# Optimization experiments

Measured on AMD Instinct MI355X. Metric: run time of the kernel, lower is better.

## Reference

```python
import jax, jax.numpy as jnp
import numpy as np

N = 50000
NEG_SLOPE = 0.2  # PyG GATConv default


def _add_self_loops(edge_index, n):
    loop = jnp.arange(n, dtype=edge_index.dtype)
    src = jnp.concatenate([edge_index[0], loop])
    dst = jnp.concatenate([edge_index[1], loop])
    return src, dst


def _gat_layer(x, src, dst, W, a_src, a_dst, b, concat):
    n = x.shape[0]
    H, C = a_src.shape
    h = (x @ W).reshape(n, H, C)                      # [N,H,C]
    s_src = jnp.sum(h * a_src, axis=-1)               # [N,H] per-node src score
    s_dst = jnp.sum(h * a_dst, axis=-1)               # [N,H] per-node dst score
    e = jax.nn.leaky_relu(s_src[src] + s_dst[dst], NEG_SLOPE)  # [E,H]
    m = jax.ops.segment_max(e, dst, num_segments=n)   # segment softmax (stable)
    ex = jnp.exp(e - m[dst])
    denom = jax.ops.segment_sum(ex, dst, num_segments=n)
    alpha = ex / denom[dst]                           # [E,H]
    out = jax.ops.segment_sum(h[src] * alpha[:, :, None], dst, num_segments=n)
    out = out.reshape(n, H * C) if concat else out.mean(axis=1)
    return out + b


def setup_inputs() -> dict:
    key = jax.random.key(0)
    ks = jax.random.split(key, 10)
    in_dim, hid, heads1, out_dim, heads2 = 256, 16, 8, 64, 1
    x = jax.random.normal(ks[0], (N, in_dim), dtype=jnp.float32)
    edge_index = jax.random.randint(ks[1], (2, 800000), 0, N, dtype=jnp.int64)
    sc1 = 1.0 / np.sqrt(in_dim)
    sc2 = 1.0 / np.sqrt(hid * heads1)
    W1 = jax.random.normal(ks[2], (in_dim, heads1 * hid), dtype=jnp.float32) * sc1
    a1_src = jax.random.normal(ks[3], (heads1, hid), dtype=jnp.float32) * sc1
    a1_dst = jax.random.normal(ks[4], (heads1, hid), dtype=jnp.float32) * sc1
    b1 = jnp.zeros((heads1 * hid,), dtype=jnp.float32)
    W2 = jax.random.normal(ks[5], (heads1 * hid, heads2 * out_dim), dtype=jnp.float32) * sc2
    a2_src = jax.random.normal(ks[6], (heads2, out_dim), dtype=jnp.float32) * sc2
    a2_dst = jax.random.normal(ks[7], (heads2, out_dim), dtype=jnp.float32) * sc2
    b2 = jnp.zeros((out_dim,), dtype=jnp.float32)
    return {"x": x, "edge_index": edge_index, "W1": W1, "a1_src": a1_src,
            "a1_dst": a1_dst, "b1": b1, "W2": W2, "a2_src": a2_src,
            "a2_dst": a2_dst, "b2": b2}


def reference(x, edge_index, W1, a1_src, a1_dst, b1, W2, a2_src, a2_dst, b2):
    # eval mode: dropout layers are identity
    src, dst = _add_self_loops(edge_index, x.shape[0])
    h = _gat_layer(x, src, dst, W1, a1_src, a1_dst, b1, concat=True)
    h = jax.nn.elu(h)
    out = _gat_layer(h, src, dst, W2, a2_src, a2_dst, b2, concat=False)
    return jax.nn.log_softmax(out, axis=1)
```

## Files before the change

### kernel.cpp

```cpp
#include <hip/hip_runtime.h>
#include <hip/hip_bf16.h>

typedef __attribute__((ext_vector_type(8))) short short8;
typedef __attribute__((ext_vector_type(4))) float f32x4;

#define EDGE_CHUNK 4096
#define CAP 128

__device__ __forceinline__ float lrelu(float v) { return fmaxf(v, 0.2f * v); }

__device__ __forceinline__ short bf16_hi(float f, float* back) {
    __hip_bfloat16 h = __float2bfloat16(f);
    *back = __bfloat162float(h);
    return __builtin_bit_cast(short, h);
}
__device__ __forceinline__ short f2bf(float f) {
    return __builtin_bit_cast(short, __float2bfloat16(f));
}


__device__ void packW_body(const float* __restrict__ W1, const float* __restrict__ a1s,
                           const float* __restrict__ a1d, const float* __restrict__ W2,
                           const float* __restrict__ a2s, const float* __restrict__ a2d,
                           short* __restrict__ w1hi, short* __restrict__ w1lo,
                           short* __restrict__ w2hi, short* __restrict__ w2lo, int t) {
    if (t < 256 * 144) {
        int j = t & 7, lane = (t >> 3) & 63, tile = t >> 9;
        int nt = tile % 9, kt = tile / 9;
        int k = kt * 32 + (lane >> 4) * 8 + j;
        int c = nt * 16 + (lane & 15);
        float w;
        if (c < 128) {
            w = W1[(size_t)k * 128 + c];
        } else {
            int hh = c - 128, h = hh & 7;
            const float* a = (hh >= 8) ? a1d : a1s;
            w = 0.f;
#pragma unroll
            for (int q = 0; q < 16; q++) w += W1[(size_t)k * 128 + h * 16 + q] * a[h * 16 + q];
        }
        float back;
        w1hi[t] = bf16_hi(w, &back);
        w1lo[t] = f2bf(w - back);
    } else {
        int u = t - 256 * 144;
        if (u >= 128 * 80) return;
        int j = u & 7, lane = (u >> 3) & 63, tile = u >> 9;
        int nt = tile % 5, kt = tile / 5;
        int k = kt * 32 + (lane >> 4) * 8 + j;
        int c = nt * 16 + (lane & 15);
        float w = 0.f;
        if (c < 64) {
            w = W2[(size_t)k * 64 + c];
        } else if (c < 66) {
            const float* a = (c == 65) ? a2d : a2s;
#pragma unroll
            for (int q = 0; q < 64; q++) w += W2[(size_t)k * 64 + q] * a[q];
        }
        float back;
        w2hi[u] = bf16_hi(w, &back);
        w2lo[u] = f2bf(w - back);
    }
}

__device__ void scatter_body(const int* __restrict__ ei, int E, int n,
                             int* __restrict__ cursor, int* __restrict__ csr_src, int vbid) {
    int slot = vbid & 7;
    int chunk = vbid >> 3;
    int lo = (int)(((long)n * slot) >> 3);
    int hi = (int)(((long)n * (slot + 1)) >> 3);
    int ET = E + n;
    int base = chunk * EDGE_CHUNK;
    int endi = min(base + EDGE_CHUNK, ET);
    for (int i = base + threadIdx.x; i < endi; i += 256) {
        int d = (i < E) ? ei[E + i] : i - E;
        if (d >= lo && d < hi) {
            int pos = atomicAdd(&cursor[d], 1);
            if (pos < CAP) {
                int s = (i < E) ? ei[i] : d;
                csr_src[(size_t)d * CAP + pos] = s;
            }
        }
    }
}

template <int K, int NT, int MODE>
__device__ void gemm_body(const float* __restrict__ A, const short* __restrict__ Bhi,
                          const short* __restrict__ Blo, unsigned short* __restrict__ hb,
                          float* __restrict__ s_s, float* __restrict__ s_d, int M, int vbid) {
    constexpr int KT = K / 32;
    constexpr int NH = NT - 1;
    __shared__ __align__(16) unsigned short stage[4][16][NH * 16];
    const int wave = threadIdx.x >> 6, lane = threadIdx.x & 63;
    const int row0 = (vbid * 4 + wave) * 16;
    if (row0 >= M) return;
    const int arow = row0 + (lane & 15);
    const float* ap = A + (size_t)arow * K + (lane >> 4) * 8;

    f32x4 acc[NT];
#pragma unroll
    for (int i = 0; i < NT; i++) acc[i] = (f32x4){0.f, 0.f, 0.f, 0.f};

    for (int kt = 0; kt < KT; kt++) {
        float av[8];
        *(float4*)(av)     = *(const float4*)(ap + kt * 32);
        *(float4*)(av + 4) = *(const float4*)(ap + kt * 32 + 4);
        short8 ahi, alo;
#pragma unroll
        for (int j = 0; j < 8; j++) {
            float back;
            ahi[j] = bf16_hi(av[j], &back);
            alo[j] = f2bf(av[j] - back);
        }
        const short8* bh = (const short8*)(Bhi + ((size_t)(kt * NT) * 64 + lane) * 8);
        const short8* bl = (const short8*)(Blo + ((size_t)(kt * NT) * 64 + lane) * 8);
#pragma unroll
        for (int nt = 0; nt < NT; nt++) {
            short8 bhv = bh[nt * 64];
            short8 blv = bl[nt * 64];
            acc[nt] = __builtin_amdgcn_mfma_f32_16x16x32_bf16(ahi, bhv, acc[nt], 0, 0, 0);
            acc[nt] = __builtin_amdgcn_mfma_f32_16x16x32_bf16(ahi, blv, acc[nt], 0, 0, 0);
            acc[nt] = __builtin_amdgcn_mfma_f32_16x16x32_bf16(alo, bhv, acc[nt], 0, 0, 0);
        }
    }
    const int rgrp = (lane >> 4) * 4;
    const int col = lane & 15;
#pragma unroll
    for (int nt = 0; nt < NH; nt++)
#pragma unroll
        for (int r = 0; r < 4; r++)
            stage[wave][rgrp + r][nt * 16 + col] = (unsigned short)f2bf(acc[nt][r]);
    asm volatile("s_waitcnt lgkmcnt(0)" ::: "memory");
    {
        const uint4* srcp = (const uint4*)&stage[wave][0][0];
        uint4* dstp = (uint4*)(hb + (size_t)row0 * (NH * 16));
#pragma unroll
        for (int c = lane; c < NH * 32; c += 64) dstp[c] = srcp[c];
    }
#pragma unroll
    for (int r = 0; r < 4; r++) {
        int orow = row0 + rgrp + r;
        float v = acc[NH][r];
        if (MODE == 1) {
            if (col < 8) s_s[orow * 8 + col] = v;
            else         s_d[orow * 8 + (col - 8)] = v;
        } else {
            if (col == 0)      s_s[orow] = v;
            else if (col == 1) s_d[orow] = v;
        }
    }
}


__launch_bounds__(256)
__global__ void fused_pack_scatter(const float* __restrict__ W1, const float* __restrict__ a1s,
                                   const float* __restrict__ a1d, const float* __restrict__ W2,
                                   const float* __restrict__ a2s, const float* __restrict__ a2d,
                                   short* __restrict__ w1hi, short* __restrict__ w1lo,
                                   short* __restrict__ w2hi, short* __restrict__ w2lo,
                                   const int* __restrict__ ei, int E, int n,
                                   int* __restrict__ cursor, int* __restrict__ csr_src,
                                   int npack) {
    if ((int)blockIdx.x < npack) {
        int t = blockIdx.x * 256 + threadIdx.x;
        packW_body(W1, a1s, a1d, W2, a2s, a2d, w1hi, w1lo, w2hi, w2lo, t);
    } else {
        scatter_body(ei, E, n, cursor, csr_src, blockIdx.x - npack);
    }
}

template <int K, int NT, int MODE>
__launch_bounds__(256)
__global__ void mfma_gemm(const float* __restrict__ A, const short* __restrict__ Bhi,
                          const short* __restrict__ Blo, unsigned short* __restrict__ hb,
                          float* __restrict__ s_s, float* __restrict__ s_d, int M) {
    gemm_body<K, NT, MODE>(A, Bhi, Blo, hb, s_s, s_d, M, blockIdx.x);
}

__launch_bounds__(256)
__global__ void gather1_kernel(const int* __restrict__ degv, const int* __restrict__ csr_src,
                               const float* __restrict__ ssrc, const float* __restrict__ sdst,
                               const unsigned short* __restrict__ h1b,
                               const float* __restrict__ b1, float* __restrict__ out1, int n) {
    int wid = blockIdx.x * 4 + (threadIdx.x >> 6);
    if (wid >= n) return;
    int lane = threadIdx.x & 63;
    int eg = lane >> 3;
    int hs = lane & 7;
    int ha = lane >> 3;
    float sd_s = sdst[wid * 8 + hs];
    int dg = degv[wid]; if (dg > CAP) dg = CAP;
    int beg = wid * CAP, end = beg + dg;
    float den_p = 0.f, a0 = 0.f, a1 = 0.f;

    int idx0 = beg + eg;
    int src_c = (idx0 < end) ? csr_src[idx0] : 0;
    int src_n = (idx0 + 8 < end) ? csr_src[idx0 + 8] : 0;
    float sc_c = (idx0 < end) ? ssrc[src_c * 8 + hs] : 0.f;

    for (int i = beg; i < end; i += 8) {
        int src_n2 = (i + 16 + eg < end) ? csr_src[i + 16 + eg] : 0;
        float sc_n = (i + 8 + eg < end) ? ssrc[src_n * 8 + hs] : 0.f;
        float e = (i + eg < end) ? __expf(lrelu(sc_c + sd_s)) : 0.f;
        den_p += e;
        int nn = end - i;
#define G1_BODY(k)                                                                  \
        {                                                                           \
            float eb = __shfl(e, (k) * 8 + ha, 64);                                 \
            int sb = __shfl(src_c, (k) * 8, 64);                                    \
            unsigned xw = *(const unsigned*)(h1b + (size_t)sb * 128 + 2 * lane);    \
            a0 = __builtin_fmaf(eb, __uint_as_float(xw << 16), a0);                 \
            a1 = __builtin_fmaf(eb, __uint_as_float(xw & 0xffff0000u), a1);         \
        }
        if (nn >= 8) {
#pragma unroll
            for (int k = 0; k < 8; k++) G1_BODY(k)
        } else {
            for (int k = 0; k < nn; k++) G1_BODY(k)
        }
#undef G1_BODY
        src_c = src_n; src_n = src_n2; sc_c = sc_n;
    }
    den_p += __shfl_xor(den_p, 8, 64);
    den_p += __shfl_xor(den_p, 16, 64);
    den_p += __shfl_xor(den_p, 32, 64);
    float den = __shfl(den_p, ha, 64);
    float inv = 1.f / den;
    float2 bb = *(const float2*)(b1 + 2 * lane);
    float o0 = __builtin_fmaf(a0, inv, bb.x);
    float o1 = __builtin_fmaf(a1, inv, bb.y);
    float2 o;
    o.x = o0 > 0.f ? o0 : (__expf(o0) - 1.f);
    o.y = o1 > 0.f ? o1 : (__expf(o1) - 1.f);
    *(float2*)(out1 + (size_t)wid * 128 + 2 * lane) = o;
}

__launch_bounds__(256)
__global__ void gather2_kernel(const int* __restrict__ degv, const int* __restrict__ csr_src,
                               const float* __restrict__ ssrc, const float* __restrict__ sdst,
                               const unsigned short* __restrict__ h2b,
                               const float* __restrict__ b2, float* __restrict__ out, int n) {
    int wid = blockIdx.x * 4 + (threadIdx.x >> 6);
    if (wid >= n) return;
    int lane = threadIdx.x & 63;
    float sd = sdst[wid];
    int dg = degv[wid]; if (dg > CAP) dg = CAP;
    int beg = wid * CAP, end = beg + dg;
    float den_p = 0.f, acc = 0.f;

    int idx0 = beg + lane;
    int src_c = (idx0 < end) ? csr_src[idx0] : 0;
    float sc_c = (idx0 < end) ? ssrc[src_c] : 0.f;

    for (int i = beg; i < end; i += 64) {
        float e = (i + lane < end) ? __expf(lrelu(sc_c + sd)) : 0.f;
        den_p += e;
        int nn = end - i; if (nn > 64) nn = 64;
#define G2_BODY(k)                                                                  \
        {                                                                           \
            float eb = __shfl(e, (k), 64);                                          \
            int sb = __shfl(src_c, (k), 64);                                        \
            float x = __uint_as_float(((unsigned)h2b[(size_t)sb * 64 + lane]) << 16);\
            acc = __builtin_fmaf(eb, x, acc);                                       \
        }
        int k = 0;
        for (; k + 8 <= nn; k += 8) {
#pragma unroll
            for (int u = 0; u < 8; u++) G2_BODY(k + u)
        }
        for (; k < nn; k++) G2_BODY(k)
#undef G2_BODY
        if (i + 64 < end) {
            int idx = i + 64 + lane;
            src_c = (idx < end) ? csr_src[idx] : 0;
            sc_c = (idx < end) ? ssrc[src_c] : 0.f;
        }
    }
#pragma unroll
    for (int off = 1; off < 64; off <<= 1) den_p += __shfl_xor(den_p, off, 64);

    float o = acc / den_p + b2[lane];
    float mx = o;
#pragma unroll
    for (int off = 32; off; off >>= 1) mx = fmaxf(mx, __shfl_xor(mx, off, 64));
    float ex = __expf(o - mx);
    float sum = ex;
#pragma unroll
    for (int off = 32; off; off >>= 1) sum += __shfl_xor(sum, off, 64);
    out[(size_t)wid * 64 + lane] = o - mx - logf(sum);
}

extern "C" void kernel_launch(void* const* d_in, const int* in_sizes, int n_in,
                              void* d_out, int out_size, void* d_ws, size_t ws_size,
                              hipStream_t stream) {
    const float* x   = (const float*)d_in[0];
    const int*   ei  = (const int*)d_in[1];
    const float* W1  = (const float*)d_in[2];
    const float* a1s = (const float*)d_in[3];
    const float* a1d = (const float*)d_in[4];
    const float* b1  = (const float*)d_in[5];
    const float* W2  = (const float*)d_in[6];
    const float* a2s = (const float*)d_in[7];
    const float* a2d = (const float*)d_in[8];
    const float* b2  = (const float*)d_in[9];
    float* out = (float*)d_out;

    const int n = in_sizes[0] / 256;
    const int E = in_sizes[1] / 2;
    const int ET = E + n;
    const int NCH = (ET + EDGE_CHUNK - 1) / EDGE_CHUNK;
    const int NPACK = (256 * 144 + 128 * 80) / 256;

    float* ws = (float*)d_ws;
    float* out1 = ws;
    float* s1s  = out1 + (size_t)n * 128;
    float* s1d  = s1s + (size_t)n * 8;
    float* s2s  = s1d + (size_t)n * 8;
    float* s2d  = s2s + n;
    unsigned short* h1b = (unsigned short*)(s2d + n);
    unsigned short* h2b = h1b + (size_t)n * 128;
    int*   cursor  = (int*)(h2b + (size_t)n * 64);
    int*   csr_src = cursor + n;
    short* w1hi    = (short*)(csr_src + (size_t)n * CAP);
    short* w1lo    = w1hi + 256 * 144;
    short* w2hi    = w1lo + 256 * 144;
    short* w2lo    = w2hi + 128 * 80;

    hipMemsetAsync(cursor, 0, (size_t)n * 4, stream);

    const int B = 256;

    fused_pack_scatter<<<NPACK + 8 * NCH, B, 0, stream>>>(W1, a1s, a1d, W2, a2s, a2d,
                                                          w1hi, w1lo, w2hi, w2lo,
                                                          ei, E, n, cursor, csr_src, NPACK);
    mfma_gemm<256, 9, 1><<<(n + 63) / 64, B, 0, stream>>>(x, w1hi, w1lo, h1b, s1s, s1d, n);
    gather1_kernel<<<(n + 3) / 4, B, 0, stream>>>(cursor, csr_src, s1s, s1d, h1b, b1, out1, n);
    mfma_gemm<128, 5, 2><<<(n + 63) / 64, B, 0, stream>>>(out1, w2hi, w2lo, h2b, s2s, s2d, n);
    gather2_kernel<<<(n + 3) / 4, B, 0, stream>>>(cursor, csr_src, s2s, s2d, h2b, b2, out, n);
}
```

Before: 259.9 us.

## Fuse layer-1 gather with layer-2 GEMM through shared memory

Merges the first-layer attention gather and the second-layer MFMA GEMM into one kernel with 1024-thread blocks covering 16 nodes. Each wave aggregates one node, splits the ELU output into bf16 hi/lo halves in shared memory, and five waves then run the 16x80 split-bf16 GEMM directly from LDS. This avoids writing and re-reading the fp32 out1 intermediate and drops one kernel launch. In exchange, blocks are large, waves 5-15 sit idle during the GEMM phase, and the block-wide barrier makes gather imbalance between nodes stall the whole block.

```diff
diff --git a/kernel.cpp b/kernel.cpp
--- a/kernel.cpp
+++ b/kernel.cpp
@@ -84,10 +84,10 @@
     }
 }
 
-template <int K, int NT, int MODE>
-__device__ void gemm_body(const float* __restrict__ A, const short* __restrict__ Bhi,
-                          const short* __restrict__ Blo, unsigned short* __restrict__ hb,
-                          float* __restrict__ s_s, float* __restrict__ s_d, int M, int vbid) {
+template <int K, int NT>
+__device__ void gemm1_body(const float* __restrict__ A, const short* __restrict__ Bhi,
+                           const short* __restrict__ Blo, unsigned short* __restrict__ hb,
+                           float* __restrict__ s_s, float* __restrict__ s_d, int M, int vbid) {
     constexpr int KT = K / 32;
     constexpr int NH = NT - 1;
     __shared__ __align__(16) unsigned short stage[4][16][NH * 16];
@@ -141,13 +141,8 @@
     for (int r = 0; r < 4; r++) {
         int orow = row0 + rgrp + r;
         float v = acc[NH][r];
-        if (MODE == 1) {
-            if (col < 8) s_s[orow * 8 + col] = v;
-            else         s_d[orow * 8 + (col - 8)] = v;
-        } else {
-            if (col == 0)      s_s[orow] = v;
-            else if (col == 1) s_d[orow] = v;
-        }
+        if (col < 8) s_s[orow * 8 + col] = v;
+        else         s_d[orow * 8 + (col - 8)] = v;
     }
 }
 
@@ -169,70 +164,126 @@
     }
 }
 
-template <int K, int NT, int MODE>
 __launch_bounds__(256)
-__global__ void mfma_gemm(const float* __restrict__ A, const short* __restrict__ Bhi,
-                          const short* __restrict__ Blo, unsigned short* __restrict__ hb,
-                          float* __restrict__ s_s, float* __restrict__ s_d, int M) {
-    gemm_body<K, NT, MODE>(A, Bhi, Blo, hb, s_s, s_d, M, blockIdx.x);
-}
-
-__launch_bounds__(256)
-__global__ void gather1_kernel(const int* __restrict__ degv, const int* __restrict__ csr_src,
-                               const float* __restrict__ ssrc, const float* __restrict__ sdst,
-                               const unsigned short* __restrict__ h1b,
-                               const float* __restrict__ b1, float* __restrict__ out1, int n) {
-    int wid = blockIdx.x * 4 + (threadIdx.x >> 6);
-    if (wid >= n) return;
-    int lane = threadIdx.x & 63;
-    int eg = lane >> 3;
-    int hs = lane & 7;
-    int ha = lane >> 3;
-    float sd_s = sdst[wid * 8 + hs];
-    int dg = degv[wid]; if (dg > CAP) dg = CAP;
-    int beg = wid * CAP, end = beg + dg;
-    float den_p = 0.f, a0 = 0.f, a1 = 0.f;
-
-    int idx0 = beg + eg;
-    int src_c = (idx0 < end) ? csr_src[idx0] : 0;
-    int src_n = (idx0 + 8 < end) ? csr_src[idx0 + 8] : 0;
-    float sc_c = (idx0 < end) ? ssrc[src_c * 8 + hs] : 0.f;
-
-    for (int i = beg; i < end; i += 8) {
-        int src_n2 = (i + 16 + eg < end) ? csr_src[i + 16 + eg] : 0;
-        float sc_n = (i + 8 + eg < end) ? ssrc[src_n * 8 + hs] : 0.f;
-        float e = (i + eg < end) ? __expf(lrelu(sc_c + sd_s)) : 0.f;
-        den_p += e;
-        int nn = end - i;
+__global__ void mfma_gemm1(const float* __restrict__ A, const short* __restrict__ Bhi,
+                           const short* __restrict__ Blo, unsigned short* __restrict__ hb,
+                           float* __restrict__ s_s, float* __restrict__ s_d, int M) {
+    gemm1_body<256, 9>(A, Bhi, Blo, hb, s_s, s_d, M, blockIdx.x);
+}
+
+__launch_bounds__(1024)
+__global__ void gather1_gemm2(const int* __restrict__ degv, const int* __restrict__ csr_src,
+                              const float* __restrict__ ssrc, const float* __restrict__ sdst,
+                              const unsigned short* __restrict__ h1b,
+                              const float* __restrict__ b1,
+                              const short* __restrict__ w2hi, const short* __restrict__ w2lo,
+                              unsigned short* __restrict__ h2b,
+                              float* __restrict__ s2s, float* __restrict__ s2d, int n) {
+    __shared__ __align__(16) unsigned short Ahi[16][136];
+    __shared__ __align__(16) unsigned short Alo[16][136];
+    __shared__ __align__(16) unsigned short hstage[16][64];
+    const int wv = threadIdx.x >> 6, lane = threadIdx.x & 63;
+    const int row0g = blockIdx.x * 16;
+    const int wid = row0g + wv;
+
+    if (wid < n) {
+        int eg = lane >> 3;
+        int hs = lane & 7;
+        int ha = lane >> 3;
+        float sd_s = sdst[wid * 8 + hs];
+        int dg = degv[wid]; if (dg > CAP) dg = CAP;
+        int beg = wid * CAP, end = beg + dg;
+        float den_p = 0.f, a0 = 0.f, a1 = 0.f;
+
+        int idx0 = beg + eg;
+        int src_c = (idx0 < end) ? csr_src[idx0] : 0;
+        int src_n = (idx0 + 8 < end) ? csr_src[idx0 + 8] : 0;
+        float sc_c = (idx0 < end) ? ssrc[src_c * 8 + hs] : 0.f;
+
+        for (int i = beg; i < end; i += 8) {
+            int src_n2 = (i + 16 + eg < end) ? csr_src[i + 16 + eg] : 0;
+            float sc_n = (i + 8 + eg < end) ? ssrc[src_n * 8 + hs] : 0.f;
+            float e = (i + eg < end) ? __expf(lrelu(sc_c + sd_s)) : 0.f;
+            den_p += e;
+            int nn = end - i;
 #define G1_BODY(k)                                                                  \
-        {                                                                           \
-            float eb = __shfl(e, (k) * 8 + ha, 64);                                 \
-            int sb = __shfl(src_c, (k) * 8, 64);                                    \
-            unsigned xw = *(const unsigned*)(h1b + (size_t)sb * 128 + 2 * lane);    \
-            a0 = __builtin_fmaf(eb, __uint_as_float(xw << 16), a0);                 \
-            a1 = __builtin_fmaf(eb, __uint_as_float(xw & 0xffff0000u), a1);         \
-        }
-        if (nn >= 8) {
-#pragma unroll
-            for (int k = 0; k < 8; k++) G1_BODY(k)
+            {                                                                       \
+                float eb = __shfl(e, (k) * 8 + ha, 64);                             \
+                int sb = __shfl(src_c, (k) * 8, 64);                                \
+                unsigned xw = *(const unsigned*)(h1b + (size_t)sb * 128 + 2 * lane);\
+                a0 = __builtin_fmaf(eb, __uint_as_float(xw << 16), a0);             \
+                a1 = __builtin_fmaf(eb, __uint_as_float(xw & 0xffff0000u), a1);     \
+            }
+            if (nn >= 8) {
+#pragma unroll
+                for (int k = 0; k < 8; k++) G1_BODY(k)
+            } else {
+                for (int k = 0; k < nn; k++) G1_BODY(k)
+            }
+#undef G1_BODY
+            src_c = src_n; src_n = src_n2; sc_c = sc_n;
+        }
+        den_p += __shfl_xor(den_p, 8, 64);
+        den_p += __shfl_xor(den_p, 16, 64);
+        den_p += __shfl_xor(den_p, 32, 64);
+        float den = __shfl(den_p, ha, 64);
+        float inv = 1.f / den;
+        float2 bb = *(const float2*)(b1 + 2 * lane);
+        float o0 = __builtin_fmaf(a0, inv, bb.x);
+        float o1 = __builtin_fmaf(a1, inv, bb.y);
+        o0 = o0 > 0.f ? o0 : (__expf(o0) - 1.f);
+        o1 = o1 > 0.f ? o1 : (__expf(o1) - 1.f);
+        float back0, back1;
+        short h0 = bf16_hi(o0, &back0);
+        short l0 = f2bf(o0 - back0);
+        short h1 = bf16_hi(o1, &back1);
+        short l1 = f2bf(o1 - back1);
+        Ahi[wv][2 * lane]     = (unsigned short)h0;
+        Ahi[wv][2 * lane + 1] = (unsigned short)h1;
+        Alo[wv][2 * lane]     = (unsigned short)l0;
+        Alo[wv][2 * lane + 1] = (unsigned short)l1;
+    }
+    __syncthreads();
+
+    if (wv < 5) {
+        const int nt = wv;
+        const int arow = lane & 15;
+        const int kq = (lane >> 4) * 8;
+        f32x4 acc = (f32x4){0.f, 0.f, 0.f, 0.f};
+#pragma unroll
+        for (int kt = 0; kt < 4; kt++) {
+            short8 ahv = *(const short8*)&Ahi[arow][kt * 32 + kq];
+            short8 alv = *(const short8*)&Alo[arow][kt * 32 + kq];
+            short8 bhv = *(const short8*)(w2hi + ((size_t)(kt * 5 + nt) * 64 + lane) * 8);
+            short8 blv = *(const short8*)(w2lo + ((size_t)(kt * 5 + nt) * 64 + lane) * 8);
+            acc = __builtin_amdgcn_mfma_f32_16x16x32_bf16(ahv, bhv, acc, 0, 0, 0);
+            acc = __builtin_amdgcn_mfma_f32_16x16x32_bf16(ahv, blv, acc, 0, 0, 0);
+            acc = __builtin_amdgcn_mfma_f32_16x16x32_bf16(alv, bhv, acc, 0, 0, 0);
+        }
+        const int rgrp = (lane >> 4) * 4;
+        const int col = lane & 15;
+        if (nt < 4) {
+#pragma unroll
+            for (int r = 0; r < 4; r++)
+                hstage[rgrp + r][nt * 16 + col] = (unsigned short)f2bf(acc[r]);
         } else {
-            for (int k = 0; k < nn; k++) G1_BODY(k)
-        }
-#undef G1_BODY
-        src_c = src_n; src_n = src_n2; sc_c = sc_n;
-    }
-    den_p += __shfl_xor(den_p, 8, 64);
-    den_p += __shfl_xor(den_p, 16, 64);
-    den_p += __shfl_xor(den_p, 32, 64);
-    float den = __shfl(den_p, ha, 64);
-    float inv = 1.f / den;
-    float2 bb = *(const float2*)(b1 + 2 * lane);
-    float o0 = __builtin_fmaf(a0, inv, bb.x);
-    float o1 = __builtin_fmaf(a1, inv, bb.y);
-    float2 o;
-    o.x = o0 > 0.f ? o0 : (__expf(o0) - 1.f);
-    o.y = o1 > 0.f ? o1 : (__expf(o1) - 1.f);
-    *(float2*)(out1 + (size_t)wid * 128 + 2 * lane) = o;
+#pragma unroll
+            for (int r = 0; r < 4; r++) {
+                int orow = row0g + rgrp + r;
+                if (orow < n) {
+                    if (col == 0)      s2s[orow] = acc[r];
+                    else if (col == 1) s2d[orow] = acc[r];
+                }
+            }
+        }
+    }
+    __syncthreads();
+    if (wv == 0) {
+        const uint4* srcp = (const uint4*)&hstage[0][0];
+        uint4* dstp = (uint4*)(h2b + (size_t)row0g * 64);
+        dstp[lane] = srcp[lane];
+        dstp[lane + 64] = srcp[lane + 64];
+    }
 }
 
 __launch_bounds__(256)
@@ -312,8 +363,7 @@
     const int NPACK = (256 * 144 + 128 * 80) / 256;
 
     float* ws = (float*)d_ws;
-    float* out1 = ws;
-    float* s1s  = out1 + (size_t)n * 128;
+    float* s1s  = ws;
     float* s1d  = s1s + (size_t)n * 8;
     float* s2s  = s1d + (size_t)n * 8;
     float* s2d  = s2s + n;
@@ -333,8 +383,8 @@
     fused_pack_scatter<<<NPACK + 8 * NCH, B, 0, stream>>>(W1, a1s, a1d, W2, a2s, a2d,
                                                           w1hi, w1lo, w2hi, w2lo,
                                                           ei, E, n, cursor, csr_src, NPACK);
-    mfma_gemm<256, 9, 1><<<(n + 63) / 64, B, 0, stream>>>(x, w1hi, w1lo, h1b, s1s, s1d, n);
-    gather1_kernel<<<(n + 3) / 4, B, 0, stream>>>(cursor, csr_src, s1s, s1d, h1b, b1, out1, n);
-    mfma_gemm<128, 5, 2><<<(n + 63) / 64, B, 0, stream>>>(out1, w2hi, w2lo, h2b, s2s, s2d, n);
+    mfma_gemm1<<<(n + 63) / 64, B, 0, stream>>>(x, w1hi, w1lo, h1b, s1s, s1d, n);
+    gather1_gemm2<<<(n + 15) / 16, 1024, 0, stream>>>(cursor, csr_src, s1s, s1d, h1b, b1,
+                                                      w2hi, w2lo, h2b, s2s, s2d, n);
     gather2_kernel<<<(n + 3) / 4, B, 0, stream>>>(cursor, csr_src, s2s, s2d, h2b, b2, out, n);
 }
```

After: 291.5 us. 12.1% more time.
